# Kernel optimization log

Measured on AMD Instinct MI355X. Metric: run time of the kernel, lower is better.

The kernel has to match this reference:

```python
import jax, jax.numpy as jnp
import numpy as np

B, C, H, W = 8, 512, 128, 128   # batch, ham_channels, feature-map H, W
S, R = 1, 64                    # md_s, md_r
EVAL_STEPS = 7
EPS = 1e-6


def conv1x1(x, w, b):
    # x: [B,C,H,W], w: [O,C] (1x1 conv kernel), b: [O]
    return jnp.einsum('bchw,oc->bohw', x, w) + b[None, :, None, None]


def _update_coef(x, bases, coef):
    # x: [B,D,N], bases: [B,D,R], coef: [B,N,R]
    num = jnp.einsum('bdn,bdr->bnr', x, bases)
    btb = jnp.einsum('bdr,bds->brs', bases, bases)          # [B,R,R]
    den = jnp.einsum('bnr,brs->bns', coef, btb)
    return coef * num / (den + EPS)


def nmf2d(x, bases):
    # Multiplicative-update NMF, eval path (inv_t = 1).
    coef = jax.nn.softmax(jnp.einsum('bdn,bdr->bnr', x, bases), axis=-1)

    def step(carry, _):
        bases, coef = carry
        coef = _update_coef(x, bases, coef)
        num = jnp.einsum('bdn,bnr->bdr', x, coef)
        ctc = jnp.einsum('bnr,bns->brs', coef, coef)        # [B,R,R]
        den = jnp.einsum('bdr,brs->bds', bases, ctc)
        bases = bases * num / (den + EPS)
        return (bases, coef), None

    (bases, coef), _ = jax.lax.scan(step, (bases, coef), None, length=EVAL_STEPS)
    coef = _update_coef(x, bases, coef)                      # compute_coef
    return jnp.einsum('bdr,bnr->bdn', bases, coef)           # bases @ coef^T


def setup_inputs() -> dict:
    key = jax.random.key(0)
    ks = jax.random.split(key, 5)
    x = jax.random.normal(ks[0], (B, C, H, W), jnp.float32)
    w_in = jax.random.normal(ks[1], (C, C), jnp.float32) * 0.02
    b_in = jnp.zeros((C,), jnp.float32)
    w_out = jax.random.normal(ks[2], (C, C), jnp.float32) * 0.02
    b_out = jnp.zeros((C,), jnp.float32)
    bases = jax.random.uniform(ks[3], (S, C // S, R), jnp.float32)
    # f.normalize(..., dim=1): L2-normalize over channel dim
    bases = bases / jnp.maximum(jnp.linalg.norm(bases, axis=1, keepdims=True), 1e-12)
    return {'x': x, 'w_in': w_in, 'b_in': b_in, 'w_out': w_out, 'b_out': b_out, 'bases': bases}


def reference(x, w_in, b_in, w_out, b_out, bases):
    # ham_in (1x1 conv) + relu
    h = jax.nn.relu(conv1x1(x, w_in, b_in))
    # NMF2D: view to [B*s, C/s, H*W], repeat bases over batch
    xf = h.reshape(B * S, C // S, H * W)
    bb = jnp.tile(bases, (B, 1, 1))                          # [B*s, C/s, R]
    y = nmf2d(xf, bb).reshape(B, C, H, W)
    # ham_out (1x1 conv, no norm) + residual relu
    y = conv1x1(y, w_out, b_out)
    return jax.nn.relu(x + y)
```

## Files before the change

kernel.cpp:

```cpp
#include <hip/hip_runtime.h>
#include <hip/hip_bf16.h>

#define B_ 8
#define C_ 512
#define N_ 16384
#define R_ 64
#define EPS 1e-6f

typedef float  f32x4  __attribute__((ext_vector_type(4)));
typedef short  bf16x4 __attribute__((ext_vector_type(4)));
typedef short  bf16x8 __attribute__((ext_vector_type(8)));

#define DI __device__ __forceinline__

DI short f2bf(float f) {
    union { float f; unsigned u; } a; a.f = f;
    unsigned r = a.u + 0x7fffu + ((a.u >> 16) & 1u);
    return (short)(r >> 16);
}
DI float bf2f(short s) {
    union { unsigned u; float f; } a;
    a.u = ((unsigned)(unsigned short)s) << 16;
    return a.f;
}
DI unsigned pk2(float lo, float hi) {
    union { __hip_bfloat162 h; unsigned u; } c;
    c.h = __float22bfloat162_rn(make_float2(lo, hi));
    return c.u;
}

union BV { bf16x8 v; bf16x4 h[2]; };
DI bf16x8 ldfrag(const short* p) {
    BV u;
    u.h[0] = *(const bf16x4*)p;
    u.h[1] = *(const bf16x4*)(p + 4);
    return u.v;
}
DI f32x4 mfma16(bf16x8 a, bf16x8 b, f32x4 c) {
    return __builtin_amdgcn_mfma_f32_16x16x32_bf16(a, b, c, 0, 0, 0);
}

__global__ __launch_bounds__(256)
void k_prep(const float* __restrict__ bases, float* __restrict__ basesT,
            short* __restrict__ basesTb, const float* __restrict__ w_in,
            short* __restrict__ wbf) {
    int idx = blockIdx.x * 256 + threadIdx.x;
    const int d = idx & 511;
    const int r = (idx >> 9) & 63;
    const float v = bases[d * 64 + r];
    basesT[idx]  = v;
    basesTb[idx] = f2bf(v);
    wbf[idx] = f2bf(w_in[idx]);
}

__global__ __launch_bounds__(256)
void k_conv1(const short* __restrict__ Wbf, const float* __restrict__ bias,
             const float* __restrict__ X, short* __restrict__ H) {
    const int nb = blockIdx.x * 128, mb = blockIdx.y * 128, bb = blockIdx.z;
    const float* Xb = X + (size_t)bb * C_ * N_;
    short* Hb = H + (size_t)bb * C_ * N_;
    __shared__ short As[128 * 36];
    __shared__ short Bs[128 * 36];
    const int t = threadIdx.x;
    const int lane = t & 63, wave = t >> 6;
    const int wm = wave >> 1, wn = wave & 1;
    const int fr = lane & 15, fg = lane >> 4;
    f32x4 zero4 = {0.f, 0.f, 0.f, 0.f};
    f32x4 acc[4][4];
    for (int i = 0; i < 4; i++) for (int j = 0; j < 4; j++) acc[i][j] = zero4;

    const int an_row = t >> 2, an_kc = (t & 3) * 8;
    const int bn = t & 15, bkp = t >> 4;

    for (int kb = 0; kb < C_; kb += 32) {
        {
#pragma unroll
            for (int i = 0; i < 2; i++) {
                const int row = an_row + 64 * i;
                const short* src = Wbf + (size_t)(mb + row) * C_ + kb + an_kc;
                short* dst = &As[row * 36 + an_kc];
                *(bf16x4*)dst = *(const bf16x4*)src;
                *(bf16x4*)(dst + 4) = *(const bf16x4*)(src + 4);
            }
        }
        {
            const float* r0 = Xb + (size_t)(kb + 2 * bkp) * N_ + nb + bn;
#pragma unroll
            for (int p = 0; p < 8; p++) {
                const float va = r0[16 * p];
                const float vb = r0[16 * p + N_];
                *(unsigned*)&Bs[(bn + 16 * p) * 36 + 2 * bkp] = pk2(va, vb);
            }
        }
        __syncthreads();
        bf16x8 af[4], bv[4];
#pragma unroll
        for (int mi = 0; mi < 4; mi++) af[mi] = ldfrag(&As[(wm * 64 + mi * 16 + fr) * 36 + fg * 8]);
#pragma unroll
        for (int ni = 0; ni < 4; ni++) bv[ni] = ldfrag(&Bs[(wn * 64 + ni * 16 + fr) * 36 + fg * 8]);
#pragma unroll
        for (int mi = 0; mi < 4; mi++)
#pragma unroll
            for (int ni = 0; ni < 4; ni++)
                acc[mi][ni] = mfma16(af[mi], bv[ni], acc[mi][ni]);
        __syncthreads();
    }
#pragma unroll
    for (int mi = 0; mi < 4; mi++) {
#pragma unroll
        for (int j = 0; j < 4; j++) {
            const int m = mb + wm * 64 + mi * 16 + fg * 4 + j;
            const float bvv = bias[m];
            short* orow = Hb + (size_t)m * N_ + nb;
#pragma unroll
            for (int ni = 0; ni < 4; ni++) {
                float v = acc[mi][ni][j] + bvv;
                v = v > 0.f ? v : 0.f;
                orow[wn * 64 + ni * 16 + fr] = f2bf(v);
            }
        }
    }
}

template<int UPDATE>
__global__ __launch_bounds__(256)
void k_coef(const short* __restrict__ basesTb, const short* __restrict__ Hh,
            const short* __restrict__ btb, short* __restrict__ coef) {
    const int nb = blockIdx.x * 256, bb = blockIdx.y;
    const short* Hb = Hh + (size_t)bb * C_ * N_;
    const short* bT = basesTb + (size_t)bb * R_ * C_;
    short* coefB = coef + (size_t)bb * R_ * N_;
    __shared__ short As[64 * 36];
    __shared__ short Bs[256 * 36];
    __shared__ short Ds[64 * 68];
    const int t = threadIdx.x;
    const int lane = t & 63, wave = t >> 6;
    const int fr = lane & 15, fg = lane >> 4;
    f32x4 zero4 = {0.f, 0.f, 0.f, 0.f};
    f32x4 accN[4][4];
    for (int i = 0; i < 4; i++) for (int j = 0; j < 4; j++) accN[i][j] = zero4;

    const int bn = 2 * (t & 15), bkp = t >> 4;

    for (int kb = 0; kb < C_; kb += 32) {
        {
            const int row = t >> 2, kc = (t & 3) * 8;
            const short* src = bT + row * C_ + kb + kc;
            short* dst = &As[row * 36 + kc];
            *(bf16x4*)dst = *(const bf16x4*)src;
            *(bf16x4*)(dst + 4) = *(const bf16x4*)(src + 4);
        }
        {
            const short* r0 = Hb + (size_t)(kb + 2 * bkp) * N_ + nb + bn;
#pragma unroll
            for (int p = 0; p < 8; p++) {
                const unsigned ra = *(const unsigned*)(r0 + 32 * p);
                const unsigned rb = *(const unsigned*)(r0 + 32 * p + N_);
                *(unsigned*)&Bs[(bn + 32 * p) * 36 + 2 * bkp] = (ra & 0xffffu) | (rb << 16);
                *(unsigned*)&Bs[(bn + 1 + 32 * p) * 36 + 2 * bkp] = (ra >> 16) | (rb & 0xffff0000u);
            }
        }
        __syncthreads();
        bf16x8 af[4], bv[4];
#pragma unroll
        for (int mi = 0; mi < 4; mi++) af[mi] = ldfrag(&As[(mi * 16 + fr) * 36 + fg * 8]);
#pragma unroll
        for (int ni = 0; ni < 4; ni++) bv[ni] = ldfrag(&Bs[(wave * 64 + ni * 16 + fr) * 36 + fg * 8]);
#pragma unroll
        for (int mi = 0; mi < 4; mi++)
#pragma unroll
            for (int ni = 0; ni < 4; ni++)
                accN[mi][ni] = mfma16(af[mi], bv[ni], accN[mi][ni]);
        __syncthreads();
    }

    f32x4 accD[4][4];
    if (UPDATE) {
        for (int i = 0; i < 4; i++) for (int j = 0; j < 4; j++) accD[i][j] = zero4;
        {
            const short* bt = btb + bb * R_ * R_;
#pragma unroll
            for (int i = 0; i < 2; i++) {
                const int row = t & 63, kc8 = ((t >> 6) + 4 * i) * 8;
                const short* src = bt + row * 64 + kc8;
                short* dst = &Ds[row * 68 + kc8];
                *(bf16x4*)dst = *(const bf16x4*)src;
                *(bf16x4*)(dst + 4) = *(const bf16x4*)(src + 4);
            }
        }
        for (int ks = 0; ks < 2; ks++) {
            const short* r0 = coefB + (size_t)(ks * 32 + 2 * bkp) * N_ + nb + bn;
#pragma unroll
            for (int p = 0; p < 8; p++) {
                const unsigned ra = *(const unsigned*)(r0 + 32 * p);
                const unsigned rb = *(const unsigned*)(r0 + 32 * p + N_);
                *(unsigned*)&Bs[(bn + 32 * p) * 36 + 2 * bkp] = (ra & 0xffffu) | (rb << 16);
                *(unsigned*)&Bs[(bn + 1 + 32 * p) * 36 + 2 * bkp] = (ra >> 16) | (rb & 0xffff0000u);
            }
            __syncthreads();
            bf16x8 af[4], bv[4];
#pragma unroll
            for (int mi = 0; mi < 4; mi++) af[mi] = ldfrag(&Ds[(mi * 16 + fr) * 68 + ks * 32 + fg * 8]);
#pragma unroll
            for (int ni = 0; ni < 4; ni++) bv[ni] = ldfrag(&Bs[(wave * 64 + ni * 16 + fr) * 36 + fg * 8]);
#pragma unroll
            for (int mi = 0; mi < 4; mi++)
#pragma unroll
                for (int ni = 0; ni < 4; ni++)
                    accD[mi][ni] = mfma16(af[mi], bv[ni], accD[mi][ni]);
            __syncthreads();
        }
#pragma unroll
        for (int mi = 0; mi < 4; mi++)
#pragma unroll
            for (int ni = 0; ni < 4; ni++)
#pragma unroll
                for (int j = 0; j < 4; j++) {
                    const int m = mi * 16 + fg * 4 + j;
                    const int n = nb + wave * 64 + ni * 16 + fr;
                    short* p = coefB + (size_t)m * N_ + n;
                    float oldv = bf2f(*p);
                    float nv = oldv * accN[mi][ni][j] / (accD[mi][ni][j] + EPS);
                    *p = f2bf(nv);
                }
    } else {
#pragma unroll
        for (int ni = 0; ni < 4; ni++) {
            float mx = -3e38f;
#pragma unroll
            for (int mi = 0; mi < 4; mi++)
#pragma unroll
                for (int j = 0; j < 4; j++) mx = fmaxf(mx, accN[mi][ni][j]);
            mx = fmaxf(mx, __shfl_xor(mx, 16, 64));
            mx = fmaxf(mx, __shfl_xor(mx, 32, 64));
            float sm = 0.f;
#pragma unroll
            for (int mi = 0; mi < 4; mi++)
#pragma unroll
                for (int j = 0; j < 4; j++) {
                    float e = __expf(accN[mi][ni][j] - mx);
                    accN[mi][ni][j] = e;
                    sm += e;
                }
            sm += __shfl_xor(sm, 16, 64);
            sm += __shfl_xor(sm, 32, 64);
            const float inv = 1.f / sm;
#pragma unroll
            for (int mi = 0; mi < 4; mi++)
#pragma unroll
                for (int j = 0; j < 4; j++) {
                    const int m = mi * 16 + fg * 4 + j;
                    const int n = nb + wave * 64 + ni * 16 + fr;
                    coefB[(size_t)m * N_ + n] = f2bf(accN[mi][ni][j] * inv);
                }
        }
    }
}

template<int MODE>
__global__ __launch_bounds__(256)
void k_tn(const short* __restrict__ coef, const short* __restrict__ Hh,
          const short* __restrict__ basesTb, const float* __restrict__ Wout,
          float* __restrict__ parts, short* __restrict__ btb, short* __restrict__ wf) {
    const int ddt = blockIdx.x, ch = blockIdx.y, bb = blockIdx.z;
    const int kLen = (MODE == 0) ? 2048 : 512;
    const int k0g = ch * kLen;
    const short* Ap; int lda;
    if (MODE == 0) { Ap = coef + (size_t)bb * R_ * N_; lda = N_; }
    else           { Ap = basesTb + (size_t)bb * R_ * C_; lda = C_; }
    __shared__ short As[64 * 68];
    __shared__ short Bs[64 * 68];
    const int t = threadIdx.x;
    const int lane = t & 63, wave = t >> 6;
    const int fr = lane & 15, fg = lane >> 4;
    f32x4 zero4 = {0.f, 0.f, 0.f, 0.f};
    f32x4 acc[4];
    for (int i = 0; i < 4; i++) acc[i] = zero4;

    for (int kb = 0; kb < kLen; kb += 64) {
#pragma unroll
        for (int i = 0; i < 2; i++) {
            const int kg = (t & 7) * 8, row = (t >> 3) + 32 * i;
            const short* src = Ap + (size_t)row * lda + k0g + kb + kg;
            short* dst = &As[row * 68 + kg];
            *(bf16x4*)dst = *(const bf16x4*)src;
            *(bf16x4*)(dst + 4) = *(const bf16x4*)(src + 4);
        }
#pragma unroll
        for (int i = 0; i < 2; i++) {
            const int kg = (t & 7) * 8, row = (t >> 3) + 32 * i;
            const int dd = ddt * 64 + row;
            short* dst = &Bs[row * 68 + kg];
            if (MODE == 2) {
                const float* src = Wout + (size_t)dd * C_ + kb + kg;
                float4 v0 = *(const float4*)src;
                float4 v1 = *(const float4*)(src + 4);
                *(unsigned*)dst = pk2(v0.x, v0.y);
                *(unsigned*)(dst + 2) = pk2(v0.z, v0.w);
                *(unsigned*)(dst + 4) = pk2(v1.x, v1.y);
                *(unsigned*)(dst + 6) = pk2(v1.z, v1.w);
            } else {
                const short* src;
                if (MODE == 0)
                    src = (dd < C_) ? Hh + (size_t)bb * C_ * N_ + (size_t)dd * N_ + k0g + kb + kg
                                    : coef + (size_t)bb * R_ * N_ + (size_t)(dd - C_) * N_ + k0g + kb + kg;
                else
                    src = basesTb + (size_t)bb * R_ * C_ + (size_t)dd * C_ + kb + kg;
                *(bf16x4*)dst = *(const bf16x4*)src;
                *(bf16x4*)(dst + 4) = *(const bf16x4*)(src + 4);
            }
        }
        __syncthreads();
#pragma unroll
        for (int kk = 0; kk < 2; kk++) {
            bf16x8 a = ldfrag(&As[(wave * 16 + fr) * 68 + kk * 32 + fg * 8]);
#pragma unroll
            for (int ni = 0; ni < 4; ni++) {
                bf16x8 b = ldfrag(&Bs[(ni * 16 + fr) * 68 + kk * 32 + fg * 8]);
                acc[ni] = mfma16(a, b, acc[ni]);
            }
        }
        __syncthreads();
    }
#pragma unroll
    for (int ni = 0; ni < 4; ni++)
#pragma unroll
        for (int j = 0; j < 4; j++) {
            const int r = wave * 16 + fg * 4 + j;
            const int dd = ddt * 64 + ni * 16 + fr;
            if (MODE == 0)
                parts[(((size_t)bb * 8 + ch) * 64 + r) * 576 + dd] = acc[ni][j];
            else if (MODE == 1)
                btb[bb * R_ * R_ + r * 64 + dd] = f2bf(acc[ni][j]);
            else
                wf[(size_t)bb * C_ * R_ + (size_t)dd * 64 + r] = f2bf(acc[ni][j]);
        }
}

__global__ __launch_bounds__(256)
void k_bases_update(const float* __restrict__ parts, float* __restrict__ basesT,
                    short* __restrict__ basesTb) {
    const int dt = blockIdx.x, bb = blockIdx.y;
    __shared__ float ctcL[64 * 64];
    const int t = threadIdx.x;
    for (int idx = t; idx < 4096; idx += 256) {
        const int r = idx >> 6, s = idx & 63;
        float sum = 0.f;
#pragma unroll
        for (int ch = 0; ch < 8; ch++)
            sum += parts[(((size_t)bb * 8 + ch) * 64 + r) * 576 + 512 + s];
        ctcL[idx] = sum;
    }
    __syncthreads();
    float nv[16];
#pragma unroll
    for (int i = 0; i < 16; i++) {
        const int idx = t + i * 256;
        const int r = idx >> 6, d = dt * 64 + (idx & 63);
        float num = 0.f;
#pragma unroll
        for (int ch = 0; ch < 8; ch++)
            num += parts[(((size_t)bb * 8 + ch) * 64 + r) * 576 + d];
        float den = 0.f;
        const float* bcol = basesT + (size_t)bb * R_ * C_ + d;
        for (int s = 0; s < 64; s++)
            den += ctcL[r * 64 + s] * bcol[(size_t)s * C_];
        const float oldv = basesT[(size_t)bb * R_ * C_ + (size_t)r * C_ + d];
        nv[i] = oldv * num / (den + EPS);
    }
    __syncthreads();
#pragma unroll
    for (int i = 0; i < 16; i++) {
        const int idx = t + i * 256;
        const int r = idx >> 6, d = dt * 64 + (idx & 63);
        basesT[(size_t)bb * R_ * C_ + (size_t)r * C_ + d] = nv[i];
        basesTb[(size_t)bb * R_ * C_ + (size_t)r * C_ + d] = f2bf(nv[i]);
    }
}

__global__ __launch_bounds__(256)
void k_final(const short* __restrict__ wf, const short* __restrict__ coef,
             const float* __restrict__ X, const float* __restrict__ bias,
             float* __restrict__ out) {
    const int nb = blockIdx.x * 128, mb = blockIdx.y * 128, bb = blockIdx.z;
    __shared__ short As[128 * 68];
    __shared__ short Bs[128 * 68];
    const int t = threadIdx.x;
    const int lane = t & 63, wave = t >> 6;
    const int wm = wave >> 1, wn = wave & 1;
    const int fr = lane & 15, fg = lane >> 4;
    const short* wfb = wf + (size_t)bb * C_ * R_;
    const short* coefB = coef + (size_t)bb * R_ * N_;
    f32x4 zero4 = {0.f, 0.f, 0.f, 0.f};
    f32x4 acc[4][4];
    for (int i = 0; i < 4; i++) for (int j = 0; j < 4; j++) acc[i][j] = zero4;

#pragma unroll
    for (int i = 0; i < 4; i++) {
        const int kg = (t & 7) * 8, row = (t >> 3) + 32 * i;
        const short* src = wfb + (size_t)(mb + row) * 64 + kg;
        short* dst = &As[row * 68 + kg];
        *(bf16x4*)dst = *(const bf16x4*)src;
        *(bf16x4*)(dst + 4) = *(const bf16x4*)(src + 4);
    }
    {
        const int bn = 2 * (t & 15), bkp = t >> 4;
#pragma unroll
        for (int i = 0; i < 2; i++) {
            const int kp = bkp + 16 * i;
            const short* r0 = coefB + (size_t)(2 * kp) * N_ + nb + bn;
#pragma unroll
            for (int p = 0; p < 4; p++) {
                const unsigned ra = *(const unsigned*)(r0 + 32 * p);
                const unsigned rb = *(const unsigned*)(r0 + 32 * p + N_);
                *(unsigned*)&Bs[(bn + 32 * p) * 68 + 2 * kp] = (ra & 0xffffu) | (rb << 16);
                *(unsigned*)&Bs[(bn + 1 + 32 * p) * 68 + 2 * kp] = (ra >> 16) | (rb & 0xffff0000u);
            }
        }
    }
    __syncthreads();
#pragma unroll
    for (int kk = 0; kk < 2; kk++) {
        bf16x8 af[4], bv[4];
#pragma unroll
        for (int mi = 0; mi < 4; mi++) af[mi] = ldfrag(&As[(wm * 64 + mi * 16 + fr) * 68 + kk * 32 + fg * 8]);
#pragma unroll
        for (int ni = 0; ni < 4; ni++) bv[ni] = ldfrag(&Bs[(wn * 64 + ni * 16 + fr) * 68 + kk * 32 + fg * 8]);
#pragma unroll
        for (int mi = 0; mi < 4; mi++)
#pragma unroll
            for (int ni = 0; ni < 4; ni++)
                acc[mi][ni] = mfma16(af[mi], bv[ni], acc[mi][ni]);
    }
    const float* Xb = X + (size_t)bb * C_ * N_;
    float* Ob = out + (size_t)bb * C_ * N_;
#pragma unroll
    for (int mi = 0; mi < 4; mi++)
#pragma unroll
        for (int j = 0; j < 4; j++) {
            const int m = mb + wm * 64 + mi * 16 + fg * 4 + j;
            const float bvv = bias[m];
            const float* xrow = Xb + (size_t)m * N_ + nb;
            float* orow = Ob + (size_t)m * N_ + nb;
#pragma unroll
            for (int ni = 0; ni < 4; ni++) {
                const int n = wn * 64 + ni * 16 + fr;
                float v = xrow[n] + acc[mi][ni][j] + bvv;
                orow[n] = v > 0.f ? v : 0.f;
            }
        }
}

extern "C" void kernel_launch(void* const* d_in, const int* in_sizes, int n_in,
                              void* d_out, int out_size, void* d_ws, size_t ws_size,
                              hipStream_t stream) {
    const float* x     = (const float*)d_in[0];
    const float* w_in  = (const float*)d_in[1];
    const float* b_in  = (const float*)d_in[2];
    const float* w_out = (const float*)d_in[3];
    const float* b_out = (const float*)d_in[4];
    const float* bases = (const float*)d_in[5];
    float* out = (float*)d_out;

    short* h       = (short*)d_ws;
    short* coef    = h + (size_t)67108864;
    float* basesT  = (float*)(coef + 8388608);
    short* basesTb = (short*)(basesT + 262144);
    short* btb     = basesTb + 262144;
    short* wf      = btb + 32768;
    float* parts   = (float*)(wf + 262144);
    short* wbf     = (short*)(parts + 2359296);

    k_prep<<<1024, 256, 0, stream>>>(bases, basesT, basesTb, w_in, wbf);
    k_conv1<<<dim3(128, 4, 8), 256, 0, stream>>>(wbf, b_in, x, h);
    k_coef<0><<<dim3(64, 8), 256, 0, stream>>>(basesTb, h, btb, coef);
    for (int s = 0; s < 7; s++) {
        k_tn<1><<<dim3(1, 1, 8), 256, 0, stream>>>(coef, h, basesTb, w_out, parts, btb, wf);
        k_coef<1><<<dim3(64, 8), 256, 0, stream>>>(basesTb, h, btb, coef);
        k_tn<0><<<dim3(9, 8, 8), 256, 0, stream>>>(coef, h, basesTb, w_out, parts, btb, wf);
        k_bases_update<<<dim3(8, 8), 256, 0, stream>>>(parts, basesT, basesTb);
    }
    k_tn<1><<<dim3(1, 1, 8), 256, 0, stream>>>(coef, h, basesTb, w_out, parts, btb, wf);
    k_coef<1><<<dim3(64, 8), 256, 0, stream>>>(basesTb, h, btb, coef);
    k_tn<2><<<dim3(8, 1, 8), 256, 0, stream>>>(coef, h, basesTb, w_out, parts, btb, wf);
    k_final<<<dim3(128, 4, 8), 256, 0, stream>>>(wf, coef, x, b_out, out);
}
```

Before: 1.473 ms.

## Store hidden activations transposed (N-major) and vectorize loads and stores across kernels

The relu'd conv1 output is now stored as [B][N][C] instead of [B][C][N]. k_coef can then load H rows contiguously with wide loads, with no bf16 repacking. MFMA operand order is swapped in k_coef and k_final so that coef and output writes become 4-wide vector stores, and conv1 reads X with float4 loads. The k_tn path that reads H now has to gather from the transposed layout with strided 4-byte loads, which may cost bandwidth in that kernel; the softmax reduction is reworked to match the new fragment layout.

```diff
diff --git a/kernel.cpp b/kernel.cpp
--- a/kernel.cpp
+++ b/kernel.cpp
@@ -55,10 +55,10 @@
 
 __global__ __launch_bounds__(256)
 void k_conv1(const short* __restrict__ Wbf, const float* __restrict__ bias,
-             const float* __restrict__ X, short* __restrict__ H) {
+             const float* __restrict__ X, short* __restrict__ Ht) {
     const int nb = blockIdx.x * 128, mb = blockIdx.y * 128, bb = blockIdx.z;
     const float* Xb = X + (size_t)bb * C_ * N_;
-    short* Hb = H + (size_t)bb * C_ * N_;
+    short* HtB = Ht + (size_t)bb * N_ * C_;
     __shared__ short As[128 * 36];
     __shared__ short Bs[128 * 36];
     const int t = threadIdx.x;
@@ -70,7 +70,7 @@
     for (int i = 0; i < 4; i++) for (int j = 0; j < 4; j++) acc[i][j] = zero4;
 
     const int an_row = t >> 2, an_kc = (t & 3) * 8;
-    const int bn = t & 15, bkp = t >> 4;
+    const int bkp = t >> 4;
 
     for (int kb = 0; kb < C_; kb += 32) {
         {
@@ -84,12 +84,17 @@
             }
         }
         {
-            const float* r0 = Xb + (size_t)(kb + 2 * bkp) * N_ + nb + bn;
-#pragma unroll
-            for (int p = 0; p < 8; p++) {
-                const float va = r0[16 * p];
-                const float vb = r0[16 * p + N_];
-                *(unsigned*)&Bs[(bn + 16 * p) * 36 + 2 * bkp] = pk2(va, vb);
+#pragma unroll
+            for (int i = 0; i < 2; i++) {
+                const int n0 = 4 * ((t & 15) + 16 * i);
+                const float* r0 = Xb + (size_t)(kb + 2 * bkp) * N_ + nb + n0;
+                float4 va = *(const float4*)r0;
+                float4 vb = *(const float4*)(r0 + N_);
+                const float* pa = (const float*)&va;
+                const float* pb = (const float*)&vb;
+#pragma unroll
+                for (int j = 0; j < 4; j++)
+                    *(unsigned*)&Bs[(n0 + j) * 36 + 2 * bkp] = pk2(pa[j], pb[j]);
             }
         }
         __syncthreads();
@@ -107,31 +112,33 @@
     }
 #pragma unroll
     for (int mi = 0; mi < 4; mi++) {
-#pragma unroll
-        for (int j = 0; j < 4; j++) {
-            const int m = mb + wm * 64 + mi * 16 + fg * 4 + j;
-            const float bvv = bias[m];
-            short* orow = Hb + (size_t)m * N_ + nb;
-#pragma unroll
-            for (int ni = 0; ni < 4; ni++) {
-                float v = acc[mi][ni][j] + bvv;
-                v = v > 0.f ? v : 0.f;
-                orow[wn * 64 + ni * 16 + fr] = f2bf(v);
-            }
+        const int c0 = mb + wm * 64 + mi * 16 + fg * 4;
+        const float4 b4 = *(const float4*)&bias[c0];
+        const float* bp = (const float*)&b4;
+#pragma unroll
+        for (int ni = 0; ni < 4; ni++) {
+            const int n = nb + wn * 64 + ni * 16 + fr;
+            bf16x4 pk;
+#pragma unroll
+            for (int j = 0; j < 4; j++) {
+                float v = acc[mi][ni][j] + bp[j];
+                pk[j] = f2bf(v > 0.f ? v : 0.f);
+            }
+            *(bf16x4*)&HtB[(size_t)n * C_ + c0] = pk;
         }
     }
 }
 
 template<int UPDATE>
 __global__ __launch_bounds__(256)
-void k_coef(const short* __restrict__ basesTb, const short* __restrict__ Hh,
+void k_coef(const short* __restrict__ basesTb, const short* __restrict__ Ht,
             const short* __restrict__ btb, short* __restrict__ coef) {
     const int nb = blockIdx.x * 256, bb = blockIdx.y;
-    const short* Hb = Hh + (size_t)bb * C_ * N_;
+    const short* HtB = Ht + (size_t)bb * N_ * C_;
     const short* bT = basesTb + (size_t)bb * R_ * C_;
     short* coefB = coef + (size_t)bb * R_ * N_;
     __shared__ short As[64 * 36];
-    __shared__ short Bs[256 * 36];
+    __shared__ short Bs[256 * 44];
     __shared__ short Ds[64 * 68];
     const int t = threadIdx.x;
     const int lane = t & 63, wave = t >> 6;
@@ -140,8 +147,6 @@
     f32x4 accN[4][4];
     for (int i = 0; i < 4; i++) for (int j = 0; j < 4; j++) accN[i][j] = zero4;
 
-    const int bn = 2 * (t & 15), bkp = t >> 4;
-
     for (int kb = 0; kb < C_; kb += 32) {
         {
             const int row = t >> 2, kc = (t & 3) * 8;
@@ -151,31 +156,31 @@
             *(bf16x4*)(dst + 4) = *(const bf16x4*)(src + 4);
         }
         {
-            const short* r0 = Hb + (size_t)(kb + 2 * bkp) * N_ + nb + bn;
-#pragma unroll
-            for (int p = 0; p < 8; p++) {
-                const unsigned ra = *(const unsigned*)(r0 + 32 * p);
-                const unsigned rb = *(const unsigned*)(r0 + 32 * p + N_);
-                *(unsigned*)&Bs[(bn + 32 * p) * 36 + 2 * bkp] = (ra & 0xffffu) | (rb << 16);
-                *(unsigned*)&Bs[(bn + 1 + 32 * p) * 36 + 2 * bkp] = (ra >> 16) | (rb & 0xffff0000u);
+            const short* src = HtB + (size_t)(nb + t) * C_ + kb;
+            short* dst = &Bs[t * 44];
+#pragma unroll
+            for (int s = 0; s < 4; s++) {
+                BV u; u.v = *(const bf16x8*)(src + 8 * s);
+                *(bf16x4*)(dst + 8 * s) = u.h[0];
+                *(bf16x4*)(dst + 8 * s + 4) = u.h[1];
             }
         }
         __syncthreads();
-        bf16x8 af[4], bv[4];
-#pragma unroll
-        for (int mi = 0; mi < 4; mi++) af[mi] = ldfrag(&As[(mi * 16 + fr) * 36 + fg * 8]);
-#pragma unroll
-        for (int ni = 0; ni < 4; ni++) bv[ni] = ldfrag(&Bs[(wave * 64 + ni * 16 + fr) * 36 + fg * 8]);
-#pragma unroll
-        for (int mi = 0; mi < 4; mi++)
-#pragma unroll
-            for (int ni = 0; ni < 4; ni++)
-                accN[mi][ni] = mfma16(af[mi], bv[ni], accN[mi][ni]);
+        bf16x8 hf[4], bfr[4];
+#pragma unroll
+        for (int nt = 0; nt < 4; nt++) hf[nt] = ldfrag(&Bs[(wave * 64 + nt * 16 + fr) * 44 + fg * 8]);
+#pragma unroll
+        for (int rt = 0; rt < 4; rt++) bfr[rt] = ldfrag(&As[(rt * 16 + fr) * 36 + fg * 8]);
+#pragma unroll
+        for (int nt = 0; nt < 4; nt++)
+#pragma unroll
+            for (int rt = 0; rt < 4; rt++)
+                accN[nt][rt] = mfma16(hf[nt], bfr[rt], accN[nt][rt]);
         __syncthreads();
     }
 
-    f32x4 accD[4][4];
     if (UPDATE) {
+        f32x4 accD[4][4];
         for (int i = 0; i < 4; i++) for (int j = 0; j < 4; j++) accD[i][j] = zero4;
         {
             const short* bt = btb + bb * R_ * R_;
@@ -189,77 +194,91 @@
             }
         }
         for (int ks = 0; ks < 2; ks++) {
-            const short* r0 = coefB + (size_t)(ks * 32 + 2 * bkp) * N_ + nb + bn;
+            const int sp = t >> 4;
+            const int s0 = ks * 32 + 2 * sp;
 #pragma unroll
             for (int p = 0; p < 8; p++) {
-                const unsigned ra = *(const unsigned*)(r0 + 32 * p);
-                const unsigned rb = *(const unsigned*)(r0 + 32 * p + N_);
-                *(unsigned*)&Bs[(bn + 32 * p) * 36 + 2 * bkp] = (ra & 0xffffu) | (rb << 16);
-                *(unsigned*)&Bs[(bn + 1 + 32 * p) * 36 + 2 * bkp] = (ra >> 16) | (rb & 0xffff0000u);
+                const int n0 = 2 * ((t & 15) + 16 * p);
+                const unsigned ra = *(const unsigned*)(coefB + (size_t)s0 * N_ + nb + n0);
+                const unsigned rb = *(const unsigned*)(coefB + (size_t)(s0 + 1) * N_ + nb + n0);
+                *(unsigned*)&Bs[n0 * 44 + 2 * sp] = (ra & 0xffffu) | (rb << 16);
+                *(unsigned*)&Bs[(n0 + 1) * 44 + 2 * sp] = (ra >> 16) | (rb & 0xffff0000u);
             }
             __syncthreads();
-            bf16x8 af[4], bv[4];
-#pragma unroll
-            for (int mi = 0; mi < 4; mi++) af[mi] = ldfrag(&Ds[(mi * 16 + fr) * 68 + ks * 32 + fg * 8]);
-#pragma unroll
-            for (int ni = 0; ni < 4; ni++) bv[ni] = ldfrag(&Bs[(wave * 64 + ni * 16 + fr) * 36 + fg * 8]);
-#pragma unroll
-            for (int mi = 0; mi < 4; mi++)
-#pragma unroll
-                for (int ni = 0; ni < 4; ni++)
-                    accD[mi][ni] = mfma16(af[mi], bv[ni], accD[mi][ni]);
+            bf16x8 cf[4], df[4];
+#pragma unroll
+            for (int nt = 0; nt < 4; nt++) cf[nt] = ldfrag(&Bs[(wave * 64 + nt * 16 + fr) * 44 + fg * 8]);
+#pragma unroll
+            for (int rt = 0; rt < 4; rt++) df[rt] = ldfrag(&Ds[(rt * 16 + fr) * 68 + ks * 32 + fg * 8]);
+#pragma unroll
+            for (int nt = 0; nt < 4; nt++)
+#pragma unroll
+                for (int rt = 0; rt < 4; rt++)
+                    accD[nt][rt] = mfma16(cf[nt], df[rt], accD[nt][rt]);
             __syncthreads();
         }
 #pragma unroll
-        for (int mi = 0; mi < 4; mi++)
-#pragma unroll
-            for (int ni = 0; ni < 4; ni++)
+        for (int nt = 0; nt < 4; nt++)
+#pragma unroll
+            for (int rt = 0; rt < 4; rt++) {
+                const int r = rt * 16 + fr;
+                const int n0 = nb + wave * 64 + nt * 16 + fg * 4;
+                short* p = coefB + (size_t)r * N_ + n0;
+                bf16x4 old = *(const bf16x4*)p;
+                bf16x4 nw;
+#pragma unroll
+                for (int j = 0; j < 4; j++)
+                    nw[j] = f2bf(bf2f(old[j]) * accN[nt][rt][j] / (accD[nt][rt][j] + EPS));
+                *(bf16x4*)p = nw;
+            }
+    } else {
+#pragma unroll
+        for (int nt = 0; nt < 4; nt++) {
+            float mx[4], sm[4];
+#pragma unroll
+            for (int j = 0; j < 4; j++) {
+                float m = accN[nt][0][j];
+#pragma unroll
+                for (int rt = 1; rt < 4; rt++) m = fmaxf(m, accN[nt][rt][j]);
+                m = fmaxf(m, __shfl_xor(m, 1, 64));
+                m = fmaxf(m, __shfl_xor(m, 2, 64));
+                m = fmaxf(m, __shfl_xor(m, 4, 64));
+                m = fmaxf(m, __shfl_xor(m, 8, 64));
+                mx[j] = m; sm[j] = 0.f;
+            }
+#pragma unroll
+            for (int rt = 0; rt < 4; rt++)
 #pragma unroll
                 for (int j = 0; j < 4; j++) {
-                    const int m = mi * 16 + fg * 4 + j;
-                    const int n = nb + wave * 64 + ni * 16 + fr;
-                    short* p = coefB + (size_t)m * N_ + n;
-                    float oldv = bf2f(*p);
-                    float nv = oldv * accN[mi][ni][j] / (accD[mi][ni][j] + EPS);
-                    *p = f2bf(nv);
+                    float e = __expf(accN[nt][rt][j] - mx[j]);
+                    accN[nt][rt][j] = e;
+                    sm[j] += e;
                 }
-    } else {
-#pragma unroll
-        for (int ni = 0; ni < 4; ni++) {
-            float mx = -3e38f;
-#pragma unroll
-            for (int mi = 0; mi < 4; mi++)
-#pragma unroll
-                for (int j = 0; j < 4; j++) mx = fmaxf(mx, accN[mi][ni][j]);
-            mx = fmaxf(mx, __shfl_xor(mx, 16, 64));
-            mx = fmaxf(mx, __shfl_xor(mx, 32, 64));
-            float sm = 0.f;
-#pragma unroll
-            for (int mi = 0; mi < 4; mi++)
-#pragma unroll
-                for (int j = 0; j < 4; j++) {
-                    float e = __expf(accN[mi][ni][j] - mx);
-                    accN[mi][ni][j] = e;
-                    sm += e;
-                }
-            sm += __shfl_xor(sm, 16, 64);
-            sm += __shfl_xor(sm, 32, 64);
-            const float inv = 1.f / sm;
-#pragma unroll
-            for (int mi = 0; mi < 4; mi++)
-#pragma unroll
-                for (int j = 0; j < 4; j++) {
-                    const int m = mi * 16 + fg * 4 + j;
-                    const int n = nb + wave * 64 + ni * 16 + fr;
-                    coefB[(size_t)m * N_ + n] = f2bf(accN[mi][ni][j] * inv);
-                }
+#pragma unroll
+            for (int j = 0; j < 4; j++) {
+                float s = sm[j];
+                s += __shfl_xor(s, 1, 64);
+                s += __shfl_xor(s, 2, 64);
+                s += __shfl_xor(s, 4, 64);
+                s += __shfl_xor(s, 8, 64);
+                sm[j] = 1.f / s;
+            }
+#pragma unroll
+            for (int rt = 0; rt < 4; rt++) {
+                const int r = rt * 16 + fr;
+                const int n0 = nb + wave * 64 + nt * 16 + fg * 4;
+                bf16x4 pk;
+#pragma unroll
+                for (int j = 0; j < 4; j++) pk[j] = f2bf(accN[nt][rt][j] * sm[j]);
+                *(bf16x4*)&coefB[(size_t)r * N_ + n0] = pk;
+            }
         }
     }
 }
 
 template<int MODE>
 __global__ __launch_bounds__(256)
-void k_tn(const short* __restrict__ coef, const short* __restrict__ Hh,
+void k_tn(const short* __restrict__ coef, const short* __restrict__ Ht,
           const short* __restrict__ basesTb, const float* __restrict__ Wout,
           float* __restrict__ parts, short* __restrict__ btb, short* __restrict__ wf) {
     const int ddt = blockIdx.x, ch = blockIdx.y, bb = blockIdx.z;
@@ -268,6 +287,7 @@
     const short* Ap; int lda;
     if (MODE == 0) { Ap = coef + (size_t)bb * R_ * N_; lda = N_; }
     else           { Ap = basesTb + (size_t)bb * R_ * C_; lda = C_; }
+    const short* HtB = Ht + (size_t)bb * N_ * C_;
     __shared__ short As[64 * 68];
     __shared__ short Bs[64 * 68];
     const int t = threadIdx.x;
@@ -286,28 +306,39 @@
             *(bf16x4*)dst = *(const bf16x4*)src;
             *(bf16x4*)(dst + 4) = *(const bf16x4*)(src + 4);
         }
-#pragma unroll
-        for (int i = 0; i < 2; i++) {
-            const int kg = (t & 7) * 8, row = (t >> 3) + 32 * i;
-            const int dd = ddt * 64 + row;
-            short* dst = &Bs[row * 68 + kg];
-            if (MODE == 2) {
-                const float* src = Wout + (size_t)dd * C_ + kb + kg;
-                float4 v0 = *(const float4*)src;
-                float4 v1 = *(const float4*)(src + 4);
-                *(unsigned*)dst = pk2(v0.x, v0.y);
-                *(unsigned*)(dst + 2) = pk2(v0.z, v0.w);
-                *(unsigned*)(dst + 4) = pk2(v1.x, v1.y);
-                *(unsigned*)(dst + 6) = pk2(v1.z, v1.w);
-            } else {
-                const short* src;
-                if (MODE == 0)
-                    src = (dd < C_) ? Hh + (size_t)bb * C_ * N_ + (size_t)dd * N_ + k0g + kb + kg
-                                    : coef + (size_t)bb * R_ * N_ + (size_t)(dd - C_) * N_ + k0g + kb + kg;
-                else
-                    src = basesTb + (size_t)bb * R_ * C_ + (size_t)dd * C_ + kb + kg;
-                *(bf16x4*)dst = *(const bf16x4*)src;
-                *(bf16x4*)(dst + 4) = *(const bf16x4*)(src + 4);
+        if (MODE == 0 && ddt < 8) {
+            const int dd0 = 2 * (t & 31);
+#pragma unroll
+            for (int i = 0; i < 4; i++) {
+                const int n0 = 2 * ((t >> 5) + 8 * i);
+                const unsigned ra = *(const unsigned*)(HtB + (size_t)(k0g + kb + n0) * C_ + ddt * 64 + dd0);
+                const unsigned rb = *(const unsigned*)(HtB + (size_t)(k0g + kb + n0 + 1) * C_ + ddt * 64 + dd0);
+                *(unsigned*)&Bs[dd0 * 68 + n0] = (ra & 0xffffu) | (rb << 16);
+                *(unsigned*)&Bs[(dd0 + 1) * 68 + n0] = (ra >> 16) | (rb & 0xffff0000u);
+            }
+        } else {
+#pragma unroll
+            for (int i = 0; i < 2; i++) {
+                const int kg = (t & 7) * 8, row = (t >> 3) + 32 * i;
+                const int dd = ddt * 64 + row;
+                short* dst = &Bs[row * 68 + kg];
+                if (MODE == 2) {
+                    const float* src = Wout + (size_t)dd * C_ + kb + kg;
+                    float4 v0 = *(const float4*)src;
+                    float4 v1 = *(const float4*)(src + 4);
+                    *(unsigned*)dst = pk2(v0.x, v0.y);
+                    *(unsigned*)(dst + 2) = pk2(v0.z, v0.w);
+                    *(unsigned*)(dst + 4) = pk2(v1.x, v1.y);
+                    *(unsigned*)(dst + 6) = pk2(v1.z, v1.w);
+                } else {
+                    const short* src;
+                    if (MODE == 0)
+                        src = coef + (size_t)bb * R_ * N_ + (size_t)(ddt * 64 + row - C_) * N_ + k0g + kb + kg;
+                    else
+                        src = basesTb + (size_t)bb * R_ * C_ + (size_t)dd * C_ + kb + kg;
+                    *(bf16x4*)dst = *(const bf16x4*)src;
+                    *(bf16x4*)(dst + 4) = *(const bf16x4*)(src + 4);
+                }
             }
         }
         __syncthreads();
@@ -322,19 +353,29 @@
         }
         __syncthreads();
     }
-#pragma unroll
-    for (int ni = 0; ni < 4; ni++)
-#pragma unroll
-        for (int j = 0; j < 4; j++) {
-            const int r = wave * 16 + fg * 4 + j;
+    if (MODE == 2) {
+#pragma unroll
+        for (int ni = 0; ni < 4; ni++) {
             const int dd = ddt * 64 + ni * 16 + fr;
-            if (MODE == 0)
-                parts[(((size_t)bb * 8 + ch) * 64 + r) * 576 + dd] = acc[ni][j];
-            else if (MODE == 1)
-                btb[bb * R_ * R_ + r * 64 + dd] = f2bf(acc[ni][j]);
-            else
-                wf[(size_t)bb * C_ * R_ + (size_t)dd * 64 + r] = f2bf(acc[ni][j]);
-        }
+            const int r0 = wave * 16 + fg * 4;
+            bf16x4 pk;
+#pragma unroll
+            for (int j = 0; j < 4; j++) pk[j] = f2bf(acc[ni][j]);
+            *(bf16x4*)&wf[(size_t)bb * C_ * R_ + (size_t)dd * 64 + r0] = pk;
+        }
+    } else {
+#pragma unroll
+        for (int ni = 0; ni < 4; ni++)
+#pragma unroll
+            for (int j = 0; j < 4; j++) {
+                const int r = wave * 16 + fg * 4 + j;
+                const int dd = ddt * 64 + ni * 16 + fr;
+                if (MODE == 0)
+                    parts[(((size_t)bb * 8 + ch) * 64 + r) * 576 + dd] = acc[ni][j];
+                else
+                    btb[bb * R_ * R_ + r * 64 + dd] = f2bf(acc[ni][j]);
+            }
+    }
 }
 
 __global__ __launch_bounds__(256)
@@ -421,34 +462,38 @@
     __syncthreads();
 #pragma unroll
     for (int kk = 0; kk < 2; kk++) {
-        bf16x8 af[4], bv[4];
+        bf16x8 cf[4], af[4];
+#pragma unroll
+        for (int ni = 0; ni < 4; ni++) cf[ni] = ldfrag(&Bs[(wn * 64 + ni * 16 + fr) * 68 + kk * 32 + fg * 8]);
 #pragma unroll
         for (int mi = 0; mi < 4; mi++) af[mi] = ldfrag(&As[(wm * 64 + mi * 16 + fr) * 68 + kk * 32 + fg * 8]);
 #pragma unroll
-        for (int ni = 0; ni < 4; ni++) bv[ni] = ldfrag(&Bs[(wn * 64 + ni * 16 + fr) * 68 + kk * 32 + fg * 8]);
-#pragma unroll
-        for (int mi = 0; mi < 4; mi++)
-#pragma unroll
-            for (int ni = 0; ni < 4; ni++)
-                acc[mi][ni] = mfma16(af[mi], bv[ni], acc[mi][ni]);
+        for (int ni = 0; ni < 4; ni++)
+#pragma unroll
+            for (int mi = 0; mi < 4; mi++)
+                acc[ni][mi] = mfma16(cf[ni], af[mi], acc[ni][mi]);
     }
     const float* Xb = X + (size_t)bb * C_ * N_;
     float* Ob = out + (size_t)bb * C_ * N_;
 #pragma unroll
-    for (int mi = 0; mi < 4; mi++)
-#pragma unroll
-        for (int j = 0; j < 4; j++) {
-            const int m = mb + wm * 64 + mi * 16 + fg * 4 + j;
-            const float bvv = bias[m];
-            const float* xrow = Xb + (size_t)m * N_ + nb;
-            float* orow = Ob + (size_t)m * N_ + nb;
-#pragma unroll
-            for (int ni = 0; ni < 4; ni++) {
-                const int n = wn * 64 + ni * 16 + fr;
-                float v = xrow[n] + acc[mi][ni][j] + bvv;
-                orow[n] = v > 0.f ? v : 0.f;
-            }
-        }
+    for (int mi = 0; mi < 4; mi++) {
+        const int m = mb + wm * 64 + mi * 16 + fr;
+        const float bvv = bias[m];
+#pragma unroll
+        for (int ni = 0; ni < 4; ni++) {
+            const int n0 = nb + wn * 64 + ni * 16 + fg * 4;
+            float4 xv = *(const float4*)&Xb[(size_t)m * N_ + n0];
+            const float* xp = (const float*)&xv;
+            float4 ov;
+            float* op = (float*)&ov;
+#pragma unroll
+            for (int j = 0; j < 4; j++) {
+                float v = xp[j] + acc[ni][mi][j] + bvv;
+                op[j] = v > 0.f ? v : 0.f;
+            }
+            *(float4*)&Ob[(size_t)m * N_ + n0] = ov;
+        }
+    }
 }
 
 extern "C" void kernel_launch(void* const* d_in, const int* in_sizes, int n_in,
@@ -462,8 +507,8 @@
     const float* bases = (const float*)d_in[5];
     float* out = (float*)d_out;
 
-    short* h       = (short*)d_ws;
-    short* coef    = h + (size_t)67108864;
+    short* ht      = (short*)d_ws;
+    short* coef    = ht + (size_t)67108864;
     float* basesT  = (float*)(coef + 8388608);
     short* basesTb = (short*)(basesT + 262144);
     short* btb     = basesTb + 262144;
@@ -472,16 +517,16 @@
     short* wbf     = (short*)(parts + 2359296);
 
     k_prep<<<1024, 256, 0, stream>>>(bases, basesT, basesTb, w_in, wbf);
-    k_conv1<<<dim3(128, 4, 8), 256, 0, stream>>>(wbf, b_in, x, h);
-    k_coef<0><<<dim3(64, 8), 256, 0, stream>>>(basesTb, h, btb, coef);
+    k_conv1<<<dim3(128, 4, 8), 256, 0, stream>>>(wbf, b_in, x, ht);
+    k_coef<0><<<dim3(64, 8), 256, 0, stream>>>(basesTb, ht, btb, coef);
     for (int s = 0; s < 7; s++) {
-        k_tn<1><<<dim3(1, 1, 8), 256, 0, stream>>>(coef, h, basesTb, w_out, parts, btb, wf);
-        k_coef<1><<<dim3(64, 8), 256, 0, stream>>>(basesTb, h, btb, coef);
-        k_tn<0><<<dim3(9, 8, 8), 256, 0, stream>>>(coef, h, basesTb, w_out, parts, btb, wf);
+        k_tn<1><<<dim3(1, 1, 8), 256, 0, stream>>>(coef, ht, basesTb, w_out, parts, btb, wf);
+        k_coef<1><<<dim3(64, 8), 256, 0, stream>>>(basesTb, ht, btb, coef);
+        k_tn<0><<<dim3(9, 8, 8), 256, 0, stream>>>(coef, ht, basesTb, w_out, parts, btb, wf);
         k_bases_update<<<dim3(8, 8), 256, 0, stream>>>(parts, basesT, basesTb);
     }
-    k_tn<1><<<dim3(1, 1, 8), 256, 0, stream>>>(coef, h, basesTb, w_out, parts, btb, wf);
-    k_coef<1><<<dim3(64, 8), 256, 0, stream>>>(basesTb, h, btb, coef);
-    k_tn<2><<<dim3(8, 1, 8), 256, 0, stream>>>(coef, h, basesTb, w_out, parts, btb, wf);
+    k_tn<1><<<dim3(1, 1, 8), 256, 0, stream>>>(coef, ht, basesTb, w_out, parts, btb, wf);
+    k_coef<1><<<dim3(64, 8), 256, 0, stream>>>(basesTb, ht, btb, coef);
+    k_tn<2><<<dim3(8, 1, 8), 256, 0, stream>>>(coef, ht, basesTb, w_out, parts, btb, wf);
     k_final<<<dim3(128, 4, 8), 256, 0, stream>>>(wf, coef, x, b_out, out);
 }
```

Measured after the change: 1.600 ms. 8.6% more time.
